# Kernel tuning notes

Hardware: AMD Instinct MI355X
Metric: run time of the kernel (lower is better)

Reference implementation:

```python
import jax, jax.numpy as jnp
import numpy as np

K = 16  # FLAGS.num_neighbors
N = 2562  # ellipsoid vertices
B = 4     # FLAGS.batch_size
M = 16384 # points per cloud
D = 3     # coordinate dim


def _mean_neighborhood(coord, pc, k):
    # coord: [N, D] query vertices; pc: [B, D, M] point cloud (channels-first)
    x2 = jnp.sum(coord * coord, axis=1)[None, :, None]          # [1, N, 1]
    y2 = jnp.sum(pc * pc, axis=1)[:, None, :]                   # [B, 1, M]
    xy = jnp.einsum('nd,bdm->bnm', coord, pc)                   # [B, N, M]
    d2 = x2 + y2 - 2.0 * xy                                     # [B, N, M]
    _, idx = jax.lax.top_k(-d2, k)                               # [B, N, K] indices into M
    Y = jnp.transpose(pc, (0, 2, 1))                             # [B, M, D]
    bv = jnp.arange(pc.shape[0])[:, None, None]                  # [B, 1, 1]
    knnY = Y[bv, idx]                                            # [B, N, K, D]
    knnY_mean = jnp.mean(knnY, axis=2)                           # [B, N, D]
    return knnY_mean[0]                                          # [N, D] (matches knnY_mean[0])


def setup_inputs() -> dict:
    key = jax.random.key(0)
    ks = jax.random.split(key, 5)
    inputs = jax.random.normal(ks[0], (N, D), dtype=jnp.float32)
    pcs = [jax.random.normal(ks[i + 1], (B, D, M), dtype=jnp.float32) for i in range(4)]
    return {"inputs": inputs, "pc0": pcs[0], "pc1": pcs[1], "pc2": pcs[2], "pc3": pcs[3]}


def reference(inputs, pc0, pc1, pc2, pc3):
    s0 = _mean_neighborhood(inputs, pc0, K)
    s1 = _mean_neighborhood(inputs, pc1, K)
    s2 = _mean_neighborhood(inputs, pc2, K)
    s3 = _mean_neighborhood(inputs, pc3, K)
    return jnp.concatenate([inputs, s0, s1, s2, s3], axis=1)  # [N, 5*D]
```

## Files before the change

kernel.cpp:

```cpp
#include <hip/hip_runtime.h>
#include <stdint.h>
#include <math.h>

#define NQ    2562
#define MPTS  16384
#define QPB   4
#define NBQ   641
#define NT    (MPTS / 256)
#define CAP   320

__global__ __launch_bounds__(256)
void passthrough_kernel(const float* __restrict__ inp, float* __restrict__ out) {
    int gid = blockIdx.x * 256 + threadIdx.x;
    if (gid < NQ * 3) {
        int n = gid / 3, c = gid - n * 3;
        out[n * 15 + c] = inp[gid];
    }
}

__device__ __forceinline__ float sqsum3(float y0, float y1, float y2) {
    return __fadd_rn(__fadd_rn(__fmul_rn(y0, y0), __fmul_rn(y1, y1)),
                     __fmul_rn(y2, y2));
}
__device__ __forceinline__ float keyf(float xs, float a2, float b2, float c2,
                                      float y0, float y1, float y2, float ysq) {
    float u = fmaf(c2, y2, fmaf(b2, y1, __fmul_rn(a2, y0)));
    return __fsub_rn(__fadd_rn(xs, ysq), u);
}
__device__ __forceinline__ unsigned long long packkey(float k, int m) {
    uint32_t kb = __float_as_uint(k);
    kb ^= (uint32_t)((int32_t)kb >> 31) | 0x80000000u;
    return ((unsigned long long)kb << 32) | (unsigned)m;
}
__device__ __forceinline__ float unmapkey(unsigned long long pk) {
    uint32_t kb = (uint32_t)(pk >> 32);
    return __uint_as_float((kb & 0x80000000u) ? (kb ^ 0x80000000u) : ~kb);
}
__device__ __forceinline__ int prefix_lt(unsigned long long m) {
    return __builtin_amdgcn_mbcnt_hi((unsigned)(m >> 32),
           __builtin_amdgcn_mbcnt_lo((unsigned)m, 0u));
}

__device__ __forceinline__ unsigned long long sort64(unsigned long long v, int lane) {
#pragma unroll
    for (int k = 2; k <= 64; k <<= 1) {
#pragma unroll
        for (int j = k >> 1; j > 0; j >>= 1) {
            unsigned long long p = __shfl_xor(v, j);
            bool up = ((lane & k) == 0) == ((lane & j) == 0);
            bool sw = up ? (p < v) : (v < p);
            v = sw ? p : v;
        }
    }
    return v;
}

__device__ __forceinline__ float rebuild_q(unsigned long long* t16p,
                                           unsigned long long* S, int& cnt,
                                           int lane, bool fin) {
    int c = cnt;
    int full = c >> 6, rem = c & 63;
    int rounds = full + ((fin && rem) ? 1 : 0);
    unsigned long long v = ~0ULL;
    for (int rd = 0; rd < rounds; ++rd) {
        int i = (rd << 6) + lane;
        unsigned long long pk = (i < c) ? S[i] : ~0ULL;
        pk = sort64(pk, lane);
        unsigned long long bsw = __shfl(pk, (31 - lane) & 63);
        v = (lane < 16) ? t16p[lane & 15] : (lane < 32) ? bsw : ~0ULL;
#pragma unroll
        for (int j = 16; j > 0; j >>= 1) {
            unsigned long long p2 = __shfl_xor(v, j);
            bool keepmin = (lane & j) == 0;
            bool less = p2 < v;
            v = (keepmin == less) ? p2 : v;
        }
        if (lane < 16) t16p[lane] = v;
    }
    if (!fin) {
        if (lane < rem) S[lane] = S[(full << 6) + lane];
        cnt = rem;
    } else {
        cnt = 0;
    }
    return unmapkey(__shfl(v, 15));
}

__global__ __launch_bounds__(256)
void ysq_kernel(const float* __restrict__ pc0, const float* __restrict__ pc1,
                const float* __restrict__ pc2, const float* __restrict__ pc3,
                float* __restrict__ ysq) {
    int gid = blockIdx.x * 256 + threadIdx.x;
    int pc = gid >> 14, m = gid & (MPTS - 1);
    const float* P = (pc == 0) ? pc0 : (pc == 1) ? pc1 : (pc == 2) ? pc2 : pc3;
    ysq[gid] = sqsum3(P[m], P[MPTS + m], P[2 * MPTS + m]);
}

template <bool USE_YSQ>
__global__ __launch_bounds__(256)
void knn_kernel(const float* __restrict__ inp,
                const float* __restrict__ pc0, const float* __restrict__ pc1,
                const float* __restrict__ pc2, const float* __restrict__ pc3,
                const float* __restrict__ ysq,
                float* __restrict__ out) {
    const int b    = blockIdx.x;
    const int wid  = threadIdx.x >> 6;
    const int lane = threadIdx.x & 63;

    const int pc = b / NBQ;
    const int nb = b - pc * NBQ;
    const float* __restrict__ P = (pc == 0) ? pc0 : (pc == 1) ? pc1
                                : (pc == 2) ? pc2 : pc3;

    __shared__ unsigned long long stk_sh[4][CAP];
    __shared__ unsigned long long t16_sh[4][16];

    if (lane < 16) t16_sh[wid][lane] = ~0ULL;

    float A2, B2, C2, XS;
    {
        int n = QPB * nb + wid;
        n = (n < NQ) ? n : (NQ - 1);
        float x0 = inp[n * 3 + 0];
        float x1 = inp[n * 3 + 1];
        float x2 = inp[n * 3 + 2];
        A2 = 2.0f * x0;
        B2 = 2.0f * x1;
        C2 = 2.0f * x2;
        XS = sqsum3(x0, x1, x2);
    }
    float tau;
    int   cnt = 0;

    const float* __restrict__ Pl = P + (lane << 2);
    const float* __restrict__ Ql = ysq + pc * MPTS + (lane << 2);

    auto push_tile = [&](int mofs, float k0, float k1, float k2, float k3) {
        unsigned long long b0 = __ballot(k0 <= tau);
        unsigned long long b1 = __ballot(k1 <= tau);
        unsigned long long b2 = __ballot(k2 <= tau);
        unsigned long long b3 = __ballot(k3 <= tau);
        int pre = prefix_lt(b0) + prefix_lt(b1) + prefix_lt(b2) + prefix_lt(b3);
        int tot = __popcll(b0) + __popcll(b1) + __popcll(b2) + __popcll(b3);
        int pos = cnt + pre;
        unsigned long long* S = stk_sh[wid];
        if (k0 <= tau) S[pos++] = packkey(k0, mofs + 0);
        if (k1 <= tau) S[pos++] = packkey(k1, mofs + 1);
        if (k2 <= tau) S[pos++] = packkey(k2, mofs + 2);
        if (k3 <= tau) S[pos++] = packkey(k3, mofs + 3);
        cnt += tot;
        if (cnt >= 64)
            tau = rebuild_q(t16_sh[wid], S, cnt, lane, false);
    };

    {
        float4 ax = *(const float4*)(Pl);
        float4 ay = *(const float4*)(Pl + MPTS);
        float4 az = *(const float4*)(Pl + 2 * MPTS);
        float q0, q1, q2, q3;
        if (USE_YSQ) {
            float4 aq = *(const float4*)(Ql);
            q0 = aq.x; q1 = aq.y; q2 = aq.z; q3 = aq.w;
        } else {
            q0 = sqsum3(ax.x, ay.x, az.x);
            q1 = sqsum3(ax.y, ay.y, az.y);
            q2 = sqsum3(ax.z, ay.z, az.z);
            q3 = sqsum3(ax.w, ay.w, az.w);
        }
        float k0 = keyf(XS, A2, B2, C2, ax.x, ay.x, az.x, q0);
        float k1 = keyf(XS, A2, B2, C2, ax.y, ay.y, az.y, q1);
        float k2 = keyf(XS, A2, B2, C2, ax.z, ay.z, az.z, q2);
        float k3 = keyf(XS, A2, B2, C2, ax.w, ay.w, az.w, q3);
        float km = fminf(fminf(k0, k1), fminf(k2, k3));
        float g = km;
        g = fminf(g, __shfl_xor(g, 1));
        g = fminf(g, __shfl_xor(g, 2));
        float m = g;
        m = fmaxf(m, __shfl_xor(m, 4));
        m = fmaxf(m, __shfl_xor(m, 8));
        m = fmaxf(m, __shfl_xor(m, 16));
        m = fmaxf(m, __shfl_xor(m, 32));
        tau = m;
        push_tile(lane << 2, k0, k1, k2, k3);
    }

    float4 cx = *(const float4*)(Pl + 256);
    float4 cy = *(const float4*)(Pl + MPTS + 256);
    float4 cz = *(const float4*)(Pl + 2 * MPTS + 256);
    float4 cq;
    if (USE_YSQ) cq = *(const float4*)(Ql + 256);

    for (int t = 1; t < NT; ++t) {
        const int tn = (t + 1 < NT) ? t + 1 : t;
        float4 nx = *(const float4*)(Pl + (tn << 8));
        float4 ny = *(const float4*)(Pl + MPTS + (tn << 8));
        float4 nz = *(const float4*)(Pl + 2 * MPTS + (tn << 8));
        float4 nq;
        if (USE_YSQ) nq = *(const float4*)(Ql + (tn << 8));

        const int mofs = (t << 8) + (lane << 2);
        float q0, q1, q2, q3;
        if (USE_YSQ) {
            q0 = cq.x; q1 = cq.y; q2 = cq.z; q3 = cq.w;
        } else {
            q0 = sqsum3(cx.x, cy.x, cz.x);
            q1 = sqsum3(cx.y, cy.y, cz.y);
            q2 = sqsum3(cx.z, cy.z, cz.z);
            q3 = sqsum3(cx.w, cy.w, cz.w);
        }
        float k0 = keyf(XS, A2, B2, C2, cx.x, cy.x, cz.x, q0);
        float k1 = keyf(XS, A2, B2, C2, cx.y, cy.y, cz.y, q1);
        float k2 = keyf(XS, A2, B2, C2, cx.z, cy.z, cz.z, q2);
        float k3 = keyf(XS, A2, B2, C2, cx.w, cy.w, cz.w, q3);
        float km = fminf(fminf(k0, k1), fminf(k2, k3));
        if (__ballot(km <= tau))
            push_tile(mofs, k0, k1, k2, k3);

        cx = nx; cy = ny; cz = nz;
        if (USE_YSQ) cq = nq;
    }

    if (cnt > 0)
        rebuild_q(t16_sh[wid], stk_sh[wid], cnt, lane, true);

    if (lane < 16) {
        unsigned long long v = t16_sh[wid][lane];
        int idx = (int)(unsigned)v;
        float gx = P[idx];
        float gy = P[MPTS + idx];
        float gz = P[2 * MPTS + idx];
#pragma unroll
        for (int off = 8; off > 0; off >>= 1) {
            gx += __shfl_down(gx, off, 16);
            gy += __shfl_down(gy, off, 16);
            gz += __shfl_down(gz, off, 16);
        }
        if (lane == 0) {
            int n = QPB * nb + wid;
            n = (n < NQ) ? n : (NQ - 1);
            float* o = out + n * 15 + 3 + 3 * pc;
            o[0] = gx * 0.0625f;
            o[1] = gy * 0.0625f;
            o[2] = gz * 0.0625f;
        }
    }
}

extern "C" void kernel_launch(void* const* d_in, const int* in_sizes, int n_in,
                              void* d_out, int out_size, void* d_ws, size_t ws_size,
                              hipStream_t stream) {
    const float* inp = (const float*)d_in[0];
    const float* pc0 = (const float*)d_in[1];
    const float* pc1 = (const float*)d_in[2];
    const float* pc2 = (const float*)d_in[3];
    const float* pc3 = (const float*)d_in[4];
    float* out = (float*)d_out;
    float* ysq = (float*)d_ws;

    hipLaunchKernelGGL(passthrough_kernel, dim3((NQ * 3 + 255) / 256), dim3(256),
                       0, stream, inp, out);

    const bool use_ysq = (ws_size >= (size_t)(4 * MPTS * sizeof(float)));
    if (use_ysq) {
        hipLaunchKernelGGL(ysq_kernel, dim3(4 * MPTS / 256), dim3(256), 0, stream,
                           pc0, pc1, pc2, pc3, ysq);
        hipLaunchKernelGGL((knn_kernel<true>), dim3(4 * NBQ), dim3(256), 0, stream,
                           inp, pc0, pc1, pc2, pc3, ysq, out);
    } else {
        hipLaunchKernelGGL((knn_kernel<false>), dim3(4 * NBQ), dim3(256), 0, stream,
                           inp, pc0, pc1, pc2, pc3, ysq, out);
    }
}
```

Baseline: 105.6 us.

## Stage point-cloud tiles cooperatively in double-buffered shared memory

Each of the four waves in a block previously loaded every tile's x, y, z (and ysq) from global memory on its own, so each block read the same data four times. Now each wave loads one channel of the tile into a double-buffered LDS array, and all waves read the shared tile. This cuts global and L2 traffic by a factor of about four. The cost is a block-wide __syncthreads every tile, which couples waves that used to run independently and that stall unevenly during rebuild_q, plus extra LDS reads and writes.

```diff
diff --git a/kernel.cpp b/kernel.cpp
--- a/kernel.cpp
+++ b/kernel.cpp
@@ -112,6 +112,7 @@
     const float* __restrict__ P = (pc == 0) ? pc0 : (pc == 1) ? pc1
                                 : (pc == 2) ? pc2 : pc3;
 
+    __shared__ float              tiles[2][4][256];
     __shared__ unsigned long long stk_sh[4][CAP];
     __shared__ unsigned long long t16_sh[4][16];
 
@@ -132,8 +133,9 @@
     float tau;
     int   cnt = 0;
 
-    const float* __restrict__ Pl = P + (lane << 2);
-    const float* __restrict__ Ql = ysq + pc * MPTS + (lane << 2);
+    const float* __restrict__ gch =
+        (wid == 0) ? P : (wid == 1) ? (P + MPTS) : (wid == 2) ? (P + 2 * MPTS)
+                   : (USE_YSQ ? (ysq + pc * MPTS) : P);
 
     auto push_tile = [&](int mofs, float k0, float k1, float k2, float k3) {
         unsigned long long b0 = __ballot(k0 <= tau);
@@ -153,71 +155,64 @@
             tau = rebuild_q(t16_sh[wid], S, cnt, lane, false);
     };
 
+    auto stage_load = [&](int t) -> float4 {
+        if (USE_YSQ || wid < 3) {
+            return *(const float4*)(gch + (t << 8) + (lane << 2));
+        } else {
+            const float* px = P + (t << 8) + (lane << 2);
+            float4 a = *(const float4*)(px);
+            float4 bq = *(const float4*)(px + MPTS);
+            float4 cq = *(const float4*)(px + 2 * MPTS);
+            float4 r;
+            r.x = sqsum3(a.x, bq.x, cq.x);
+            r.y = sqsum3(a.y, bq.y, cq.y);
+            r.z = sqsum3(a.z, bq.z, cq.z);
+            r.w = sqsum3(a.w, bq.w, cq.w);
+            return r;
+        }
+    };
+
     {
-        float4 ax = *(const float4*)(Pl);
-        float4 ay = *(const float4*)(Pl + MPTS);
-        float4 az = *(const float4*)(Pl + 2 * MPTS);
-        float q0, q1, q2, q3;
-        if (USE_YSQ) {
-            float4 aq = *(const float4*)(Ql);
-            q0 = aq.x; q1 = aq.y; q2 = aq.z; q3 = aq.w;
-        } else {
-            q0 = sqsum3(ax.x, ay.x, az.x);
-            q1 = sqsum3(ax.y, ay.y, az.y);
-            q2 = sqsum3(ax.z, ay.z, az.z);
-            q3 = sqsum3(ax.w, ay.w, az.w);
-        }
-        float k0 = keyf(XS, A2, B2, C2, ax.x, ay.x, az.x, q0);
-        float k1 = keyf(XS, A2, B2, C2, ax.y, ay.y, az.y, q1);
-        float k2 = keyf(XS, A2, B2, C2, ax.z, ay.z, az.z, q2);
-        float k3 = keyf(XS, A2, B2, C2, ax.w, ay.w, az.w, q3);
+        float4 s0 = stage_load(0);
+        *(float4*)&tiles[0][wid][lane << 2] = s0;
+    }
+    __syncthreads();
+
+    for (int t = 0; t < NT; ++t) {
+        const int cur = t & 1;
+        float4 stg;
+        if (t + 1 < NT) stg = stage_load(t + 1);
+
+        float4 xv = *(const float4*)&tiles[cur][0][lane << 2];
+        float4 yv = *(const float4*)&tiles[cur][1][lane << 2];
+        float4 zv = *(const float4*)&tiles[cur][2][lane << 2];
+        float4 qv = *(const float4*)&tiles[cur][3][lane << 2];
+
+        const int mofs = (t << 8) + (lane << 2);
+        float k0 = keyf(XS, A2, B2, C2, xv.x, yv.x, zv.x, qv.x);
+        float k1 = keyf(XS, A2, B2, C2, xv.y, yv.y, zv.y, qv.y);
+        float k2 = keyf(XS, A2, B2, C2, xv.z, yv.z, zv.z, qv.z);
+        float k3 = keyf(XS, A2, B2, C2, xv.w, yv.w, zv.w, qv.w);
         float km = fminf(fminf(k0, k1), fminf(k2, k3));
-        float g = km;
-        g = fminf(g, __shfl_xor(g, 1));
-        g = fminf(g, __shfl_xor(g, 2));
-        float m = g;
-        m = fmaxf(m, __shfl_xor(m, 4));
-        m = fmaxf(m, __shfl_xor(m, 8));
-        m = fmaxf(m, __shfl_xor(m, 16));
-        m = fmaxf(m, __shfl_xor(m, 32));
-        tau = m;
-        push_tile(lane << 2, k0, k1, k2, k3);
-    }
-
-    float4 cx = *(const float4*)(Pl + 256);
-    float4 cy = *(const float4*)(Pl + MPTS + 256);
-    float4 cz = *(const float4*)(Pl + 2 * MPTS + 256);
-    float4 cq;
-    if (USE_YSQ) cq = *(const float4*)(Ql + 256);
-
-    for (int t = 1; t < NT; ++t) {
-        const int tn = (t + 1 < NT) ? t + 1 : t;
-        float4 nx = *(const float4*)(Pl + (tn << 8));
-        float4 ny = *(const float4*)(Pl + MPTS + (tn << 8));
-        float4 nz = *(const float4*)(Pl + 2 * MPTS + (tn << 8));
-        float4 nq;
-        if (USE_YSQ) nq = *(const float4*)(Ql + (tn << 8));
-
-        const int mofs = (t << 8) + (lane << 2);
-        float q0, q1, q2, q3;
-        if (USE_YSQ) {
-            q0 = cq.x; q1 = cq.y; q2 = cq.z; q3 = cq.w;
-        } else {
-            q0 = sqsum3(cx.x, cy.x, cz.x);
-            q1 = sqsum3(cx.y, cy.y, cz.y);
-            q2 = sqsum3(cx.z, cy.z, cz.z);
-            q3 = sqsum3(cx.w, cy.w, cz.w);
-        }
-        float k0 = keyf(XS, A2, B2, C2, cx.x, cy.x, cz.x, q0);
-        float k1 = keyf(XS, A2, B2, C2, cx.y, cy.y, cz.y, q1);
-        float k2 = keyf(XS, A2, B2, C2, cx.z, cy.z, cz.z, q2);
-        float k3 = keyf(XS, A2, B2, C2, cx.w, cy.w, cz.w, q3);
-        float km = fminf(fminf(k0, k1), fminf(k2, k3));
-        if (__ballot(km <= tau))
+
+        if (t == 0) {
+            float g = km;
+            g = fminf(g, __shfl_xor(g, 1));
+            g = fminf(g, __shfl_xor(g, 2));
+            float m = g;
+            m = fmaxf(m, __shfl_xor(m, 4));
+            m = fmaxf(m, __shfl_xor(m, 8));
+            m = fmaxf(m, __shfl_xor(m, 16));
+            m = fmaxf(m, __shfl_xor(m, 32));
+            tau = m;
             push_tile(mofs, k0, k1, k2, k3);
-
-        cx = nx; cy = ny; cz = nz;
-        if (USE_YSQ) cq = nq;
+        } else if (__ballot(km <= tau)) {
+            push_tile(mofs, k0, k1, k2, k3);
+        }
+
+        if (t + 1 < NT) *(float4*)&tiles[cur ^ 1][wid][lane << 2] = stg;
+
+        __syncthreads();
     }
 
     if (cnt > 0)
```

After: 128.5 us. 1.22x slower.
